# Optimization experiments

Hardware: AMD Instinct MI355X
Metric: run time of the kernel (lower is better)

Reference implementation:

```python
import jax, jax.numpy as jnp
import numpy as np

B, HW, D = 16, 3600, 512
LC, NL = 768, 20
KC, VC, H = 512, 512, 8
EPS = 1e-5


def instance_norm(x):
    # x: [B, N, C]; InstanceNorm1d normalizes over the length dim N per (sample, channel),
    # biased variance, no affine (torch default).
    mu = jnp.mean(x, axis=1, keepdims=True)
    var = jnp.mean((x - mu) ** 2, axis=1, keepdims=True)
    return (x - mu) / jnp.sqrt(var + EPS)


def setup_inputs() -> dict:
    key = jax.random.key(0)
    ks = jax.random.split(key, 16)
    x = jax.random.normal(ks[0], (B, HW, D), dtype=jnp.float32)
    l = jax.random.normal(ks[1], (B, LC, NL), dtype=jnp.float32)
    # 0/1 padding mask; guarantee at least the first token is valid
    lengths = jax.random.randint(ks[2], (B, 1), 5, NL + 1)
    l_mask = (jnp.arange(NL)[None, :] < lengths).astype(jnp.float32)[:, :, None]  # [B,NL,1]
    s = 0.02
    params = dict(
        Wvis=jax.random.normal(ks[3], (D, D)) * s, bvis=jnp.zeros((D,)),
        Wq=jax.random.normal(ks[4], (KC, D)) * s, bq=jnp.zeros((KC,)),
        Wk=jax.random.normal(ks[5], (KC, LC)) * s, bk=jnp.zeros((KC,)),
        Wval=jax.random.normal(ks[6], (VC, LC)) * s, bval=jnp.zeros((VC,)),
        Ww=jax.random.normal(ks[7], (VC, VC)) * s, bw=jnp.zeros((VC,)),
        Wmm=jax.random.normal(ks[8], (VC, VC)) * s, bmm=jnp.zeros((VC,)),
    )
    return {"x": x, "l": l, "l_mask": l_mask, **params}


def reference(x, l, l_mask, Wvis, bvis, Wq, bq, Wk, bk, Wval, bval, Ww, bw, Wmm, bmm):
    b, hw, d = x.shape
    mask = l_mask[..., 0][:, None, :]  # [B,1,NL]
    # vis branch: Conv1d(dim,dim,1) + GELU (exact) + Dropout(0)
    vis = jax.nn.gelu(x @ Wvis.T + bvis, approximate=False)  # [B,HW,D]
    # query: Conv1d(v_in,KC,1) then InstanceNorm1d over HW
    q = instance_norm(x @ Wq.T + bq)  # [B,HW,KC]
    # key/value: Conv1d over language channels, then mask
    k = (jnp.einsum('kc,bcn->bkn', Wk, l) + bk[None, :, None]) * mask    # [B,KC,NL]
    v = (jnp.einsum('vc,bcn->bvn', Wval, l) + bval[None, :, None]) * mask  # [B,VC,NL]
    qh = q.reshape(b, hw, H, KC // H).transpose(0, 2, 1, 3)   # [B,H,HW,KC/H]
    kh = k.reshape(b, H, KC // H, NL)                         # [B,H,KC/H,NL]
    vh = v.reshape(b, H, VC // H, NL)                         # [B,H,VC/H,NL]
    sim = jnp.einsum('bhqd,bhdn->bhqn', qh, kh) * (KC ** -0.5)
    sim = sim + (10000.0 * mask[:, :, None, :] - 10000.0)     # additive mask bias
    attn = jax.nn.softmax(sim, axis=-1)
    out = jnp.einsum('bhqn,bhdn->bhqd', attn, vh)             # [B,H,HW,VC/H]
    out = out.transpose(0, 2, 1, 3).reshape(b, hw, VC)
    lang = instance_norm(out @ Ww.T + bw)                     # W: Conv1d + IN over HW
    mm = jax.nn.gelu((vis * lang) @ Wmm.T + bmm, approximate=False)
    return mm  # [B,HW,VC]
```

## Files before the change

### kernel.cpp

```cpp
#include <hip/hip_runtime.h>


#define B_   16
#define HW_  3600
#define D_   512
#define LC_  768
#define NL_  20

typedef __attribute__((ext_vector_type(8))) __bf16 bf16x8;
typedef __attribute__((ext_vector_type(4))) float f32x4;
typedef __attribute__((ext_vector_type(4))) float float4v;
typedef __attribute__((ext_vector_type(8))) unsigned short ushort8v;
typedef __attribute__((ext_vector_type(4))) unsigned short ushort4v;
typedef __attribute__((ext_vector_type(2))) unsigned int uint2v;

static __device__ __forceinline__ float bf2f(unsigned short u){
  unsigned int x = ((unsigned int)u) << 16; float f;
  __builtin_memcpy(&f, &x, 4); return f;
}
static __device__ __forceinline__ unsigned short f2bf(float f){
  unsigned int x; __builtin_memcpy(&x, &f, 4);
  x += 0x7fffu + ((x >> 16) & 1u);
  return (unsigned short)(x >> 16);
}
static __device__ __forceinline__ unsigned int pack2bf(float lo, float hi){
  return (unsigned int)f2bf(lo) | ((unsigned int)f2bf(hi) << 16);
}
static __device__ __forceinline__ float gelu_f(float x){
  float z  = x * 0.7071067811865476f;
  float az = fabsf(z);
  float t = 1.0f / fmaf(0.3275911f, az, 1.0f);
  float p = fmaf(1.061405429f, t, -1.453152027f);
  p = fmaf(p, t, 1.421413741f);
  p = fmaf(p, t, -0.284496736f);
  p = fmaf(p, t, 0.254829592f);
  p = p * t;
  float er = 1.0f - p * __expf(-az * az);
  er = copysignf(er, z);
  return 0.5f * x * (1.0f + er);
}

__global__ void k_cvt(const float* __restrict__ src, unsigned short* __restrict__ dst, int n4){
  int i = blockIdx.x * 256 + threadIdx.x;
  int stride = gridDim.x * 256;
  for (; i < n4; i += stride){
    float4v v = ((const float4v*)src)[i];
    ushort4v u;
    u.x = f2bf(v.x); u.y = f2bf(v.y); u.z = f2bf(v.z); u.w = f2bf(v.w);
    ((ushort4v*)dst)[i] = u;
  }
}

__global__ void k_kv(const float* __restrict__ l, const float* __restrict__ l_mask,
                     const float* __restrict__ Wk, const float* __restrict__ bk,
                     const float* __restrict__ Wval, const float* __restrict__ bval,
                     float* __restrict__ k_s, float* __restrict__ v_s){
  const int b = blockIdx.y;
  const int part = blockIdx.x;
  const bool isK = part < 8;
  const int c0 = (part & 7) * 64;
  const float* W  = isK ? Wk : Wval;
  const float* bi = isK ? bk : bval;
  float* outp = isK ? k_s : v_s;

  __shared__ float l_sh[LC_ * NL_];
  for (int i = threadIdx.x; i < LC_ * NL_; i += 256)
    l_sh[i] = l[(size_t)b * LC_ * NL_ + i];
  __syncthreads();

  const int tid = threadIdx.x;
  const int cl = tid >> 2;
  const int q  = tid & 3;
  const int c  = c0 + cl;
  const float* wrow = W + (size_t)c * LC_;
  float acc[5] = {0.f,0.f,0.f,0.f,0.f};
  for (int i = 0; i < LC_; ++i){
    float wv = wrow[i];
    const float* lr = l_sh + i * NL_ + q * 5;
    acc[0] = fmaf(wv, lr[0], acc[0]);
    acc[1] = fmaf(wv, lr[1], acc[1]);
    acc[2] = fmaf(wv, lr[2], acc[2]);
    acc[3] = fmaf(wv, lr[3], acc[3]);
    acc[4] = fmaf(wv, lr[4], acc[4]);
  }
  const float bb = bi[c];
  #pragma unroll
  for (int n5 = 0; n5 < 5; ++n5){
    int n = q * 5 + n5;
    float m = l_mask[b * NL_ + n];
    float val = (acc[n5] + bb) * m;
    if (isK) val *= 0.04419417382415922f;
    outp[((size_t)b * 512 + c) * NL_ + n] = val;
  }
}

template<int MODE, int NT, bool STATS>
__global__ __launch_bounds__(256, 4) void k_gemm(
    const unsigned short* __restrict__ A,
    const unsigned short* __restrict__ Bm,
    const float* __restrict__ bias0, const float* __restrict__ bias1,
    unsigned short* __restrict__ o0, unsigned short* __restrict__ o1,
    float* __restrict__ of, float2* __restrict__ partial)
{
  __shared__ __align__(16) unsigned short sA[2][128 * 32];
  __shared__ __align__(16) unsigned short sB[2][128 * 32];
  __shared__ float2 red[2][128];

  const int nwg = 29 * NT * B_;
  const int per = nwg >> 3;
  const int d = blockIdx.x;
  const int g = (d & 7) * per + (d >> 3);
  constexpr int NSH = (NT == 8) ? 3 : 2;
  const int nt = g & (NT - 1);
  const int rem = g >> NSH;
  const int mt = rem % 29;
  const int b  = rem / 29;

  const int m0 = mt * 128;
  const int n0 = nt * 128;
  const int tid = threadIdx.x;
  const int w = tid >> 6, lane = tid & 63;
  const int wr = w >> 1, wc = w & 1;
  const int mvalid = HW_ - m0;
  const unsigned short* Ab = A + (size_t)b * HW_ * 512;

  f32x4 acc[4][4];
  #pragma unroll
  for (int i = 0; i < 4; ++i)
    #pragma unroll
    for (int j = 0; j < 4; ++j)
      acc[i][j] = (f32x4){0.f, 0.f, 0.f, 0.f};

  auto stage = [&](int kt, int buf){
    const int k0 = kt * 32;
    #pragma unroll
    for (int s = 0; s < 2; ++s){
      int chunk = s * 256 + tid;
      int row = chunk >> 2, part = chunk & 3;
      int psrc = part ^ ((row >> 1) & 3);
      int grow = row < mvalid ? row : (mvalid - 1);
      const unsigned short* gsrc = Ab + ((size_t)(m0 + grow) * 512 + k0 + psrc * 8);
      unsigned short* ldst = &sA[buf][(s * 256 + w * 64) * 8];
      __builtin_amdgcn_global_load_lds((const __attribute__((address_space(1))) void*)gsrc,
                                       (__attribute__((address_space(3))) void*)ldst, 16, 0, 0);
    }
    #pragma unroll
    for (int s = 0; s < 2; ++s){
      int chunk = s * 256 + tid;
      int row = chunk >> 2, part = chunk & 3;
      int psrc = part ^ ((row >> 1) & 3);
      const unsigned short* gsrc = Bm + ((size_t)(n0 + row) * 512 + k0 + psrc * 8);
      unsigned short* ldst = &sB[buf][(s * 256 + w * 64) * 8];
      __builtin_amdgcn_global_load_lds((const __attribute__((address_space(1))) void*)gsrc,
                                       (__attribute__((address_space(3))) void*)ldst, 16, 0, 0);
    }
  };

  auto compute = [&](int buf){
    const unsigned short* lA = &sA[buf][(wr * 64) * 32];
    const unsigned short* lB = &sB[buf][(wc * 64) * 32];
    const int r = lane & 15, kb = lane >> 4;
    const int kx = (kb ^ ((r >> 1) & 3)) * 8;
    bf16x8 av[4], bv[4];
    #pragma unroll
    for (int i = 0; i < 4; ++i) av[i] = *(const bf16x8*)(lA + (i * 16 + r) * 32 + kx);
    #pragma unroll
    for (int j = 0; j < 4; ++j) bv[j] = *(const bf16x8*)(lB + (j * 16 + r) * 32 + kx);
    #pragma unroll
    for (int i = 0; i < 4; ++i)
      #pragma unroll
      for (int j = 0; j < 4; ++j)
        acc[i][j] = __builtin_amdgcn_mfma_f32_16x16x32_bf16(av[i], bv[j], acc[i][j], 0, 0, 0);
  };

  stage(0, 0);
  #pragma unroll
  for (int t = 0; t < 16; ++t){
    asm volatile("s_waitcnt lgkmcnt(0)" ::: "memory");
    __builtin_amdgcn_sched_barrier(0);
    asm volatile("s_waitcnt vmcnt(0)" ::: "memory");
    __builtin_amdgcn_s_barrier();
    __builtin_amdgcn_sched_barrier(0);
    if (t < 15) stage(t + 1, (t + 1) & 1);
    compute(t & 1);
  }

  int cols[4]; float bsv[4];
  #pragma unroll
  for (int j = 0; j < 4; ++j){
    int col = n0 + wc * 64 + j * 16 + (lane & 15);
    cols[j] = col;
    if (MODE == 0) bsv[j] = (col < 512) ? bias0[col] : bias1[col - 512];
    else           bsv[j] = bias0[col];
  }
  const bool do_stats = STATS && (MODE != 0 || n0 >= 512);
  float colsum[4] = {0.f,0.f,0.f,0.f}, colsq[4] = {0.f,0.f,0.f,0.f};

  #pragma unroll
  for (int i = 0; i < 4; ++i){
    int rowb = m0 + wr * 64 + i * 16 + (lane >> 4) * 4;
    #pragma unroll
    for (int rr = 0; rr < 4; ++rr){
      int row = rowb + rr;
      if (row < HW_){
        size_t rb = ((size_t)b * HW_ + row) * 512;
        #pragma unroll
        for (int j = 0; j < 4; ++j){
          float v = acc[i][j][rr] + bsv[j];
          if (MODE == 0){
            if (cols[j] < 512) o0[rb + cols[j]]       = f2bf(gelu_f(v));
            else               o1[rb + cols[j] - 512] = f2bf(v);
          } else if (MODE == 1){
            o0[rb + cols[j]] = f2bf(v);
          } else {
            of[rb + cols[j]] = gelu_f(v);
          }
          if (STATS && do_stats){
            colsum[j] += v;
            colsq[j]  = fmaf(v, v, colsq[j]);
          }
        }
      }
    }
  }

  if (STATS){
    #pragma unroll
    for (int j = 0; j < 4; ++j){
      colsum[j] += __shfl_xor(colsum[j], 16);
      colsum[j] += __shfl_xor(colsum[j], 32);
      colsq[j]  += __shfl_xor(colsq[j], 16);
      colsq[j]  += __shfl_xor(colsq[j], 32);
    }
    if ((lane >> 4) == 0 && do_stats){
      #pragma unroll
      for (int j = 0; j < 4; ++j)
        red[wr][wc * 64 + j * 16 + (lane & 15)] = make_float2(colsum[j], colsq[j]);
    }
    __syncthreads();
    if (tid < 128 && do_stats){
      float2 r0 = red[0][tid], r1 = red[1][tid];
      int gcol = n0 + tid - (MODE == 0 ? 512 : 0);
      partial[((size_t)b * 29 + mt) * 512 + gcol] = make_float2(r0.x + r1.x, r0.y + r1.y);
    }
  }
}

__global__ void k_stats_p2b(const float2* __restrict__ partial, float2* __restrict__ stats){
  const int b = blockIdx.x;
  const int c = threadIdx.x;
  float s = 0.f, q = 0.f;
  for (int mt = 0; mt < 29; ++mt){
    float2 p = partial[((size_t)b * 29 + mt) * 512 + c];
    s += p.x; q += p.y;
  }
  float mean = s * (1.0f / (float)HW_);
  float var  = q * (1.0f / (float)HW_) - mean * mean;
  stats[(size_t)b * 512 + c] = make_float2(mean, rsqrtf(var + 1e-5f));
}

__global__ void k_prep(const float* __restrict__ k_s, const float* __restrict__ v_s,
                       const float2* __restrict__ stats, const float* __restrict__ l_mask,
                       unsigned short* __restrict__ k2, unsigned short* __restrict__ v2,
                       float* __restrict__ e_s)
{
  const int b = blockIdx.x;
  const int tid = threadIdx.x;
  __shared__ float wred[4][NL_];

  float part[NL_];
  #pragma unroll
  for (int n = 0; n < NL_; ++n) part[n] = 0.f;
  #pragma unroll
  for (int half = 0; half < 2; ++half){
    int c = tid + half * 256;
    float2 st = stats[(size_t)b * 512 + c];
    float ms = st.x * st.y;
    const float* row = k_s + ((size_t)b * 512 + c) * NL_;
    #pragma unroll
    for (int n = 0; n < NL_; ++n) part[n] = fmaf(ms, row[n], part[n]);
  }
  #pragma unroll
  for (int n = 0; n < NL_; ++n){
    float v = part[n];
    v += __shfl_xor(v, 1);  v += __shfl_xor(v, 2);  v += __shfl_xor(v, 4);
    v += __shfl_xor(v, 8);  v += __shfl_xor(v, 16); v += __shfl_xor(v, 32);
    part[n] = v;
  }
  if ((tid & 63) == 0){
    #pragma unroll
    for (int n = 0; n < NL_; ++n) wred[tid >> 6][n] = part[n];
  }
  __syncthreads();
  if (tid < 32){
    float e;
    if (tid < NL_){
      float d = wred[0][tid] + wred[1][tid] + wred[2][tid] + wred[3][tid];
      e = -d - 10000.0f * (1.0f - l_mask[b * NL_ + tid]);
    } else {
      e = -1e30f;
    }
    e_s[b * 32 + tid] = e;
  }

  for (int i = tid; i < 16384; i += 256){
    int h = i >> 11, t = (i >> 10) & 1, s = (i >> 9) & 1;
    int l = (i >> 3) & 63, j = i & 7;
    int r = l & 15, g = l >> 4;
    int n = t * 16 + r;
    int c = h * 64 + s * 32 + g * 8 + j;
    unsigned short val = 0;
    if (n < NL_){
      float inv = stats[(size_t)b * 512 + c].y;
      val = f2bf(inv * k_s[((size_t)b * 512 + c) * NL_ + n]);
    }
    k2[(size_t)b * 16384 + i] = val;
  }
  for (int i = tid; i < 16384; i += 256){
    int h = i >> 11, ct = (i >> 9) & 3;
    int l = (i >> 3) & 63, j = i & 7;
    int r = l & 15, g = l >> 4;
    int n = g * 8 + j;
    int c = h * 64 + ct * 16 + r;
    unsigned short val = 0;
    if (n < NL_) val = f2bf(v_s[((size_t)b * 512 + c) * NL_ + n]);
    v2[(size_t)b * 16384 + i] = val;
  }
}

__global__ __launch_bounds__(256) void k_attn2(unsigned short* __restrict__ qraw,
    const unsigned short* __restrict__ k2, const unsigned short* __restrict__ v2,
    const float* __restrict__ e_s)
{
  const int b = blockIdx.y;
  const int w = threadIdx.x >> 6;
  const int tile = blockIdx.x * 4 + w;
  __shared__ __align__(16) unsigned short p_sh[4][16 * 32];
  __shared__ __align__(16) unsigned short o_sh[4][16 * 72];
  if (tile >= 225) return;
  const int lane = threadIdx.x & 63;
  const int r = lane & 15, g = lane >> 4;
  const int row0 = tile * 16;

  float4v e0 = *(const float4v*)(e_s + b * 32 + g * 4);
  float4v e1 = *(const float4v*)(e_s + b * 32 + 16 + g * 4);

  bf16x8 qf[8][2];
  const unsigned short* qbase = qraw + ((size_t)(b * HW_ + row0 + r) * 512) + g * 8;
  #pragma unroll
  for (int h = 0; h < 8; ++h)
    #pragma unroll
    for (int s = 0; s < 2; ++s)
      qf[h][s] = *(const bf16x8*)(qbase + h * 64 + s * 32);

  const unsigned short* kb = k2 + (size_t)b * 16384 + lane * 8;
  const unsigned short* vb = v2 + (size_t)b * 16384 + lane * 8;
  unsigned short* psh = &p_sh[w][0];
  unsigned short* osh = &o_sh[w][0];

  for (int h = 0; h < 8; ++h){
    bf16x8 kf00 = *(const bf16x8*)(kb + (h * 4 + 0) * 512);
    bf16x8 kf01 = *(const bf16x8*)(kb + (h * 4 + 1) * 512);
    bf16x8 kf10 = *(const bf16x8*)(kb + (h * 4 + 2) * 512);
    bf16x8 kf11 = *(const bf16x8*)(kb + (h * 4 + 3) * 512);
    f32x4 c0 = (f32x4){0.f,0.f,0.f,0.f};
    f32x4 c1 = (f32x4){0.f,0.f,0.f,0.f};
    c0 = __builtin_amdgcn_mfma_f32_16x16x32_bf16(kf00, qf[h][0], c0, 0, 0, 0);
    c0 = __builtin_amdgcn_mfma_f32_16x16x32_bf16(kf01, qf[h][1], c0, 0, 0, 0);
    c1 = __builtin_amdgcn_mfma_f32_16x16x32_bf16(kf10, qf[h][0], c1, 0, 0, 0);
    c1 = __builtin_amdgcn_mfma_f32_16x16x32_bf16(kf11, qf[h][1], c1, 0, 0, 0);

    float l0[4], l1[4];
    #pragma unroll
    for (int i = 0; i < 4; ++i){ l0[i] = c0[i] + e0[i]; l1[i] = c1[i] + e1[i]; }
    float m = fmaxf(fmaxf(fmaxf(l0[0], l0[1]), fmaxf(l0[2], l0[3])),
                    fmaxf(fmaxf(l1[0], l1[1]), fmaxf(l1[2], l1[3])));
    m = fmaxf(m, __shfl_xor(m, 16));
    m = fmaxf(m, __shfl_xor(m, 32));
    float p0[4], p1[4];
    #pragma unroll
    for (int i = 0; i < 4; ++i){ p0[i] = __expf(l0[i] - m); p1[i] = __expf(l1[i] - m); }

    uint2v pw0, pw1;
    pw0.x = pack2bf(p0[0], p0[1]); pw0.y = pack2bf(p0[2], p0[3]);
    pw1.x = pack2bf(p1[0], p1[1]); pw1.y = pack2bf(p1[2], p1[3]);
    float sum = bf2f((unsigned short)(pw0.x & 0xffff)) + bf2f((unsigned short)(pw0.x >> 16))
              + bf2f((unsigned short)(pw0.y & 0xffff)) + bf2f((unsigned short)(pw0.y >> 16))
              + bf2f((unsigned short)(pw1.x & 0xffff)) + bf2f((unsigned short)(pw1.x >> 16))
              + bf2f((unsigned short)(pw1.y & 0xffff)) + bf2f((unsigned short)(pw1.y >> 16));
    sum += __shfl_xor(sum, 16);
    sum += __shfl_xor(sum, 32);
    float inv = 1.0f / sum;

    *(uint2v*)(psh + r * 32 + 4 * g)      = pw0;
    *(uint2v*)(psh + r * 32 + 16 + 4 * g) = pw1;
    bf16x8 pfrag = *(const bf16x8*)(psh + r * 32 + g * 8);

    f32x4 dd[4];
    #pragma unroll
    for (int ct = 0; ct < 4; ++ct){
      bf16x8 vf = *(const bf16x8*)(vb + (h * 4 + ct) * 512);
      f32x4 z = (f32x4){0.f,0.f,0.f,0.f};
      dd[ct] = __builtin_amdgcn_mfma_f32_16x16x32_bf16(vf, pfrag, z, 0, 0, 0);
    }
    #pragma unroll
    for (int ct = 0; ct < 4; ++ct){
      uint2v ow;
      ow.x = pack2bf(dd[ct][0] * inv, dd[ct][1] * inv);
      ow.y = pack2bf(dd[ct][2] * inv, dd[ct][3] * inv);
      *(uint2v*)(osh + r * 72 + ct * 16 + 4 * g) = ow;
    }
    int frow = lane >> 2, fch = lane & 3;
    ushort8v t0 = *(const ushort8v*)(osh + frow * 72 + fch * 16);
    ushort8v t1 = *(const ushort8v*)(osh + frow * 72 + fch * 16 + 8);
    unsigned short* gdst = qraw + ((size_t)(b * HW_ + row0 + frow) * 512) + h * 64 + fch * 16;
    *(ushort8v*)(gdst)     = t0;
    *(ushort8v*)(gdst + 8) = t1;
  }
}

__global__ __launch_bounds__(256) void k_hmul(unsigned short* __restrict__ yw,
    const unsigned short* __restrict__ visb, const float2* __restrict__ stats)
{
  const int b = blockIdx.y, blk = blockIdx.x;
  const int w = threadIdx.x >> 6, lane = threadIdx.x & 63;
  const int c0 = lane * 8;
  float mean[8], inv[8];
  #pragma unroll
  for (int j = 0; j < 8; ++j){
    float2 st = stats[(size_t)b * 512 + c0 + j];
    mean[j] = st.x; inv[j] = st.y;
  }
  for (int it = 0; it < 30; ++it){
    int row = blk * 120 + it * 4 + w;
    size_t off = ((size_t)b * HW_ + row) * 512 + c0;
    ushort8v yv = *(const ushort8v*)(yw + off);
    ushort8v vv = *(const ushort8v*)(visb + off);
    ushort8v hv;
    #pragma unroll
    for (int j = 0; j < 8; ++j){
      float lang = (bf2f(yv[j]) - mean[j]) * inv[j];
      hv[j] = f2bf(bf2f(vv[j]) * lang);
    }
    *(ushort8v*)(yw + off) = hv;
  }
}

extern "C" void kernel_launch(void* const* d_in, const int* in_sizes, int n_in,
                              void* d_out, int out_size, void* d_ws, size_t ws_size,
                              hipStream_t stream)
{
  const float* x     = (const float*)d_in[0];
  const float* l     = (const float*)d_in[1];
  const float* lmask = (const float*)d_in[2];
  const float* Wvis  = (const float*)d_in[3];
  const float* bvis  = (const float*)d_in[4];
  const float* Wq    = (const float*)d_in[5];
  const float* bq    = (const float*)d_in[6];
  const float* Wk    = (const float*)d_in[7];
  const float* bk    = (const float*)d_in[8];
  const float* Wval  = (const float*)d_in[9];
  const float* bval  = (const float*)d_in[10];
  const float* Ww    = (const float*)d_in[11];
  const float* bw    = (const float*)d_in[12];
  const float* Wmm   = (const float*)d_in[13];
  const float* bmm   = (const float*)d_in[14];
  float* out = (float*)d_out;

  char* ws = (char*)d_ws;
  if (ws_size < 240517120ull) return;
  unsigned short* xb    = (unsigned short*)(ws + 0);
  unsigned short* visb  = (unsigned short*)(ws + 58982400);
  unsigned short* qraw  = (unsigned short*)(ws + 117964800);
  unsigned short* yw    = (unsigned short*)(ws + 176947200);
  unsigned short* wcat  = (unsigned short*)(ws + 235929600);
  unsigned short* wwb   = (unsigned short*)(ws + 236978176);
  unsigned short* wmmb  = (unsigned short*)(ws + 237502464);
  float*  k_s    = (float*)(ws + 238026752);
  float*  v_s    = (float*)(ws + 238682112);
  float2* stats_q= (float2*)(ws + 240386048);
  float2* stats_w= (float2*)(ws + 240451584);
  unsigned short* k2 = (unsigned short*)(ws + 0);
  unsigned short* v2 = (unsigned short*)(ws + 524288);
  float*          e_s = (float*)(ws + 1048576);
  float2* partial_q = (float2*)(ws + 176947200);
  float2* partial_w = (float2*)(ws + 1052672);

  k_cvt<<<2048, 256, 0, stream>>>(x, xb, (B_ * HW_ * D_) / 4);
  k_cvt<<<256, 256, 0, stream>>>(Wvis, wcat, (512 * 512) / 4);
  k_cvt<<<256, 256, 0, stream>>>(Wq, wcat + 262144, (512 * 512) / 4);
  k_cvt<<<256, 256, 0, stream>>>(Ww, wwb, (512 * 512) / 4);
  k_cvt<<<256, 256, 0, stream>>>(Wmm, wmmb, (512 * 512) / 4);

  k_kv<<<dim3(16, B_), 256, 0, stream>>>(l, lmask, Wk, bk, Wval, bval, k_s, v_s);

  k_gemm<0, 8, true><<<29 * 8 * B_, 256, 0, stream>>>(xb, wcat, bvis, bq, visb, qraw, nullptr, partial_q);

  k_stats_p2b<<<B_, 512, 0, stream>>>(partial_q, stats_q);

  k_prep<<<B_, 256, 0, stream>>>(k_s, v_s, stats_q, lmask, k2, v2, e_s);

  k_attn2<<<dim3(57, B_), 256, 0, stream>>>(qraw, k2, v2, e_s);

  k_gemm<1, 4, true><<<29 * 4 * B_, 256, 0, stream>>>(qraw, wwb, bw, nullptr, yw, nullptr, nullptr, partial_w);

  k_stats_p2b<<<B_, 512, 0, stream>>>(partial_w, stats_w);

  k_hmul<<<dim3(30, B_), 256, 0, stream>>>(yw, visb, stats_w);

  k_gemm<2, 4, false><<<29 * 4 * B_, 256, 0, stream>>>(yw, wmmb, bmm, nullptr, nullptr, nullptr, out, nullptr);
}
```

Baseline: 424.0 us.

## Stage GEMM epilogue through LDS for vectorized stores; merge convert and stats launches

The GEMM epilogue now writes each wave's output tile into the reused shared-memory buffers and then issues wide 16-byte row-contiguous global stores. Before, each lane scattered scalar 2- or 4-byte stores. The five fp32-to-bf16 convert launches become one kernel, and the query instance-norm stats reduction is folded into k_prep, which drops a launch. The cost is extra LDS traffic and a barrier in the epilogue, plus a serial 29-way partial reduction inside k_prep.

After: 387.1 us. 1.1x faster.

```diff
diff --git a/kernel.cpp b/kernel.cpp
--- a/kernel.cpp
+++ b/kernel.cpp
@@ -40,14 +40,32 @@
   return 0.5f * x * (1.0f + er);
 }
 
-__global__ void k_cvt(const float* __restrict__ src, unsigned short* __restrict__ dst, int n4){
+__global__ void k_cvt_all(const float* __restrict__ x,
+                          const float* __restrict__ Wvis, const float* __restrict__ Wq,
+                          const float* __restrict__ Ww,   const float* __restrict__ Wmm,
+                          unsigned short* __restrict__ xb, unsigned short* __restrict__ wcat,
+                          unsigned short* __restrict__ wwb, unsigned short* __restrict__ wmmb){
+  const int NX4 = (B_ * HW_ * D_) / 4;
+  const int TOT = NX4 + 4 * 65536;
   int i = blockIdx.x * 256 + threadIdx.x;
   int stride = gridDim.x * 256;
-  for (; i < n4; i += stride){
-    float4v v = ((const float4v*)src)[i];
+  for (; i < TOT; i += stride){
+    const float4v* s; ushort4v* dp;
+    if (i < NX4){
+      s  = (const float4v*)x + i;
+      dp = (ushort4v*)xb + i;
+    } else {
+      int k = i - NX4;
+      int seg = k >> 16, o = k & 0xFFFF;
+      if      (seg == 0){ s = (const float4v*)Wvis + o; dp = (ushort4v*)wcat + o; }
+      else if (seg == 1){ s = (const float4v*)Wq   + o; dp = (ushort4v*)wcat + 65536 + o; }
+      else if (seg == 2){ s = (const float4v*)Ww   + o; dp = (ushort4v*)wwb + o; }
+      else              { s = (const float4v*)Wmm  + o; dp = (ushort4v*)wmmb + o; }
+    }
+    float4v v = *s;
     ushort4v u;
     u.x = f2bf(v.x); u.y = f2bf(v.y); u.z = f2bf(v.z); u.w = f2bf(v.w);
-    ((ushort4v*)dst)[i] = u;
+    *dp = u;
   }
 }
 
@@ -102,8 +120,7 @@
     unsigned short* __restrict__ o0, unsigned short* __restrict__ o1,
     float* __restrict__ of, float2* __restrict__ partial)
 {
-  __shared__ __align__(16) unsigned short sA[2][128 * 32];
-  __shared__ __align__(16) unsigned short sB[2][128 * 32];
+  __shared__ __align__(16) unsigned short smem[2][2][128 * 32];
   __shared__ float2 red[2][128];
 
   const int nwg = 29 * NT * B_;
@@ -121,6 +138,7 @@
   const int tid = threadIdx.x;
   const int w = tid >> 6, lane = tid & 63;
   const int wr = w >> 1, wc = w & 1;
+  const int lr_ = lane & 15, lg_ = lane >> 4;
   const int mvalid = HW_ - m0;
   const unsigned short* Ab = A + (size_t)b * HW_ * 512;
 
@@ -140,7 +158,7 @@
       int psrc = part ^ ((row >> 1) & 3);
       int grow = row < mvalid ? row : (mvalid - 1);
       const unsigned short* gsrc = Ab + ((size_t)(m0 + grow) * 512 + k0 + psrc * 8);
-      unsigned short* ldst = &sA[buf][(s * 256 + w * 64) * 8];
+      unsigned short* ldst = &smem[0][buf][(s * 256 + w * 64) * 8];
       __builtin_amdgcn_global_load_lds((const __attribute__((address_space(1))) void*)gsrc,
                                        (__attribute__((address_space(3))) void*)ldst, 16, 0, 0);
     }
@@ -150,22 +168,21 @@
       int row = chunk >> 2, part = chunk & 3;
       int psrc = part ^ ((row >> 1) & 3);
       const unsigned short* gsrc = Bm + ((size_t)(n0 + row) * 512 + k0 + psrc * 8);
-      unsigned short* ldst = &sB[buf][(s * 256 + w * 64) * 8];
+      unsigned short* ldst = &smem[1][buf][(s * 256 + w * 64) * 8];
       __builtin_amdgcn_global_load_lds((const __attribute__((address_space(1))) void*)gsrc,
                                        (__attribute__((address_space(3))) void*)ldst, 16, 0, 0);
     }
   };
 
   auto compute = [&](int buf){
-    const unsigned short* lA = &sA[buf][(wr * 64) * 32];
-    const unsigned short* lB = &sB[buf][(wc * 64) * 32];
-    const int r = lane & 15, kb = lane >> 4;
-    const int kx = (kb ^ ((r >> 1) & 3)) * 8;
+    const unsigned short* lA = &smem[0][buf][(wr * 64) * 32];
+    const unsigned short* lB = &smem[1][buf][(wc * 64) * 32];
+    const int kx = (lg_ ^ ((lr_ >> 1) & 3)) * 8;
     bf16x8 av[4], bv[4];
     #pragma unroll
-    for (int i = 0; i < 4; ++i) av[i] = *(const bf16x8*)(lA + (i * 16 + r) * 32 + kx);
-    #pragma unroll
-    for (int j = 0; j < 4; ++j) bv[j] = *(const bf16x8*)(lB + (j * 16 + r) * 32 + kx);
+    for (int i = 0; i < 4; ++i) av[i] = *(const bf16x8*)(lA + (i * 16 + lr_) * 32 + kx);
+    #pragma unroll
+    for (int j = 0; j < 4; ++j) bv[j] = *(const bf16x8*)(lB + (j * 16 + lr_) * 32 + kx);
     #pragma unroll
     for (int i = 0; i < 4; ++i)
       #pragma unroll
@@ -185,46 +202,33 @@
     compute(t & 1);
   }
 
-  int cols[4]; float bsv[4];
+  const int colbase = n0 + wc * 64;
+  float bsv[4];
   #pragma unroll
   for (int j = 0; j < 4; ++j){
-    int col = n0 + wc * 64 + j * 16 + (lane & 15);
-    cols[j] = col;
+    int col = colbase + j * 16 + lr_;
     if (MODE == 0) bsv[j] = (col < 512) ? bias0[col] : bias1[col - 512];
     else           bsv[j] = bias0[col];
   }
   const bool do_stats = STATS && (MODE != 0 || n0 >= 512);
-  float colsum[4] = {0.f,0.f,0.f,0.f}, colsq[4] = {0.f,0.f,0.f,0.f};
-
-  #pragma unroll
-  for (int i = 0; i < 4; ++i){
-    int rowb = m0 + wr * 64 + i * 16 + (lane >> 4) * 4;
-    #pragma unroll
-    for (int rr = 0; rr < 4; ++rr){
-      int row = rowb + rr;
-      if (row < HW_){
-        size_t rb = ((size_t)b * HW_ + row) * 512;
-        #pragma unroll
-        for (int j = 0; j < 4; ++j){
-          float v = acc[i][j][rr] + bsv[j];
-          if (MODE == 0){
-            if (cols[j] < 512) o0[rb + cols[j]]       = f2bf(gelu_f(v));
-            else               o1[rb + cols[j] - 512] = f2bf(v);
-          } else if (MODE == 1){
-            o0[rb + cols[j]] = f2bf(v);
-          } else {
-            of[rb + cols[j]] = gelu_f(v);
-          }
-          if (STATS && do_stats){
+
+  if (STATS && do_stats){
+    float colsum[4] = {0.f,0.f,0.f,0.f}, colsq[4] = {0.f,0.f,0.f,0.f};
+    #pragma unroll
+    for (int i = 0; i < 4; ++i){
+      int rowb = m0 + wr * 64 + i * 16 + lg_ * 4;
+      #pragma unroll
+      for (int rr = 0; rr < 4; ++rr){
+        if (rowb + rr < HW_){
+          #pragma unroll
+          for (int j = 0; j < 4; ++j){
+            float v = acc[i][j][rr] + bsv[j];
             colsum[j] += v;
             colsq[j]  = fmaf(v, v, colsq[j]);
           }
         }
       }
     }
-  }
-
-  if (STATS){
     #pragma unroll
     for (int j = 0; j < 4; ++j){
       colsum[j] += __shfl_xor(colsum[j], 16);
@@ -232,16 +236,67 @@
       colsq[j]  += __shfl_xor(colsq[j], 16);
       colsq[j]  += __shfl_xor(colsq[j], 32);
     }
-    if ((lane >> 4) == 0 && do_stats){
+    if (lg_ == 0){
       #pragma unroll
       for (int j = 0; j < 4; ++j)
-        red[wr][wc * 64 + j * 16 + (lane & 15)] = make_float2(colsum[j], colsq[j]);
-    }
-    __syncthreads();
-    if (tid < 128 && do_stats){
-      float2 r0 = red[0][tid], r1 = red[1][tid];
-      int gcol = n0 + tid - (MODE == 0 ? 512 : 0);
-      partial[((size_t)b * 29 + mt) * 512 + gcol] = make_float2(r0.x + r1.x, r0.y + r1.y);
+        red[wr][wc * 64 + j * 16 + lr_] = make_float2(colsum[j], colsq[j]);
+    }
+  }
+
+  __syncthreads();
+
+  if (STATS && do_stats && tid < 128){
+    float2 r0 = red[0][tid], r1 = red[1][tid];
+    int gcol = n0 + tid - (MODE == 0 ? 512 : 0);
+    partial[((size_t)b * 29 + mt) * 512 + gcol] = make_float2(r0.x + r1.x, r0.y + r1.y);
+  }
+
+  unsigned short* stw = &smem[0][0][0] + w * 4096;
+
+  if (MODE == 2){
+    float* stgf = (float*)stw;
+    #pragma unroll
+    for (int half = 0; half < 2; ++half){
+      #pragma unroll
+      for (int i2 = 0; i2 < 2; ++i2){
+        int i = half * 2 + i2;
+        #pragma unroll
+        for (int rr = 0; rr < 4; ++rr)
+          #pragma unroll
+          for (int j = 0; j < 4; ++j)
+            stgf[(i2 * 16 + lg_ * 4 + rr) * 64 + j * 16 + lr_] = gelu_f(acc[i][j][rr] + bsv[j]);
+      }
+      #pragma unroll
+      for (int pass = 0; pass < 8; ++pass){
+        int chunk = pass * 64 + lane;
+        int row = chunk >> 4, sub = chunk & 15;
+        float4v vv = *(const float4v*)(stgf + row * 64 + sub * 4);
+        int grow = m0 + wr * 64 + half * 32 + row;
+        if (grow < HW_)
+          *(float4v*)(of + ((size_t)b * HW_ + grow) * 512 + colbase + sub * 4) = vv;
+      }
+    }
+  } else {
+    const bool isg = (MODE == 0) && (n0 < 512);
+    #pragma unroll
+    for (int i = 0; i < 4; ++i)
+      #pragma unroll
+      for (int rr = 0; rr < 4; ++rr)
+        #pragma unroll
+        for (int j = 0; j < 4; ++j){
+          float v = acc[i][j][rr] + bsv[j];
+          stw[(i * 16 + lg_ * 4 + rr) * 64 + j * 16 + lr_] = f2bf(isg ? gelu_f(v) : v);
+        }
+    unsigned short* optr = (MODE == 1 || isg) ? o0 : o1;
+    const int coloff = (MODE == 1 || isg) ? colbase : (colbase - 512);
+    #pragma unroll
+    for (int pass = 0; pass < 8; ++pass){
+      int chunk = pass * 64 + lane;
+      int row = chunk >> 3, sub = chunk & 7;
+      ushort8v vv = *(const ushort8v*)(stw + row * 64 + sub * 8);
+      int grow = m0 + wr * 64 + row;
+      if (grow < HW_)
+        *(ushort8v*)(optr + ((size_t)b * HW_ + grow) * 512 + coloff + sub * 8) = vv;
     }
   }
 }
@@ -259,22 +314,37 @@
   stats[(size_t)b * 512 + c] = make_float2(mean, rsqrtf(var + 1e-5f));
 }
 
-__global__ void k_prep(const float* __restrict__ k_s, const float* __restrict__ v_s,
-                       const float2* __restrict__ stats, const float* __restrict__ l_mask,
+__global__ void k_prep(const float2* __restrict__ partial, const float* __restrict__ k_s,
+                       const float* __restrict__ v_s, const float* __restrict__ l_mask,
                        unsigned short* __restrict__ k2, unsigned short* __restrict__ v2,
                        float* __restrict__ e_s)
 {
   const int b = blockIdx.x;
   const int tid = threadIdx.x;
   __shared__ float wred[4][NL_];
-
-  float part[NL_];
-  #pragma unroll
-  for (int n = 0; n < NL_; ++n) part[n] = 0.f;
+  __shared__ float2 stats_sh[512];
+
   #pragma unroll
   for (int half = 0; half < 2; ++half){
     int c = tid + half * 256;
-    float2 st = stats[(size_t)b * 512 + c];
+    float s = 0.f, q = 0.f;
+    for (int mt = 0; mt < 29; ++mt){
+      float2 p = partial[((size_t)b * 29 + mt) * 512 + c];
+      s += p.x; q += p.y;
+    }
+    float mean = s * (1.0f / (float)HW_);
+    float var  = q * (1.0f / (float)HW_) - mean * mean;
+    stats_sh[c] = make_float2(mean, rsqrtf(var + 1e-5f));
+  }
+  __syncthreads();
+
+  float part[NL_];
+  #pragma unroll
+  for (int n = 0; n < NL_; ++n) part[n] = 0.f;
+  #pragma unroll
+  for (int half = 0; half < 2; ++half){
+    int c = tid + half * 256;
+    float2 st = stats_sh[c];
     float ms = st.x * st.y;
     const float* row = k_s + ((size_t)b * 512 + c) * NL_;
     #pragma unroll
@@ -295,8 +365,8 @@
   if (tid < 32){
     float e;
     if (tid < NL_){
-      float d = wred[0][tid] + wred[1][tid] + wred[2][tid] + wred[3][tid];
-      e = -d - 10000.0f * (1.0f - l_mask[b * NL_ + tid]);
+      float dsum = wred[0][tid] + wred[1][tid] + wred[2][tid] + wred[3][tid];
+      e = -dsum - 10000.0f * (1.0f - l_mask[b * NL_ + tid]);
     } else {
       e = -1e30f;
     }
@@ -311,7 +381,7 @@
     int c = h * 64 + s * 32 + g * 8 + j;
     unsigned short val = 0;
     if (n < NL_){
-      float inv = stats[(size_t)b * 512 + c].y;
+      float inv = stats_sh[c].y;
       val = f2bf(inv * k_s[((size_t)b * 512 + c) * NL_ + n]);
     }
     k2[(size_t)b * 16384 + i] = val;
@@ -478,7 +548,6 @@
   unsigned short* wmmb  = (unsigned short*)(ws + 237502464);
   float*  k_s    = (float*)(ws + 238026752);
   float*  v_s    = (float*)(ws + 238682112);
-  float2* stats_q= (float2*)(ws + 240386048);
   float2* stats_w= (float2*)(ws + 240451584);
   unsigned short* k2 = (unsigned short*)(ws + 0);
   unsigned short* v2 = (unsigned short*)(ws + 524288);
@@ -486,19 +555,13 @@
   float2* partial_q = (float2*)(ws + 176947200);
   float2* partial_w = (float2*)(ws + 1052672);
 
-  k_cvt<<<2048, 256, 0, stream>>>(x, xb, (B_ * HW_ * D_) / 4);
-  k_cvt<<<256, 256, 0, stream>>>(Wvis, wcat, (512 * 512) / 4);
-  k_cvt<<<256, 256, 0, stream>>>(Wq, wcat + 262144, (512 * 512) / 4);
-  k_cvt<<<256, 256, 0, stream>>>(Ww, wwb, (512 * 512) / 4);
-  k_cvt<<<256, 256, 0, stream>>>(Wmm, wmmb, (512 * 512) / 4);
+  k_cvt_all<<<2048, 256, 0, stream>>>(x, Wvis, Wq, Ww, Wmm, xb, wcat, wwb, wmmb);
 
   k_kv<<<dim3(16, B_), 256, 0, stream>>>(l, lmask, Wk, bk, Wval, bval, k_s, v_s);
 
   k_gemm<0, 8, true><<<29 * 8 * B_, 256, 0, stream>>>(xb, wcat, bvis, bq, visb, qraw, nullptr, partial_q);
 
-  k_stats_p2b<<<B_, 512, 0, stream>>>(partial_q, stats_q);
-
-  k_prep<<<B_, 256, 0, stream>>>(k_s, v_s, stats_q, lmask, k2, v2, e_s);
+  k_prep<<<B_, 256, 0, stream>>>(partial_q, k_s, v_s, lmask, k2, v2, e_s);
 
   k_attn2<<<dim3(57, B_), 256, 0, stream>>>(qraw, k2, v2, e_s);
 
```
